# Kernel tuning notes

Hardware: AMD Instinct MI355X
Metric: run time of the kernel (lower is better)

Reference implementation:

```python
import jax, jax.numpy as jnp
import numpy as np
from math import sqrt

B, N, DIM_IN, DIM_K, DIM_V, NH = 4, 1024, 1024, 1024, 1024, 16


def setup_inputs() -> dict:
    key = jax.random.key(0)
    ks = jax.random.split(key, 5)
    x = jax.random.normal(ks[0], (B, N, DIM_IN), dtype=jnp.float32)
    y = jax.random.normal(ks[1], (B, N, DIM_IN), dtype=jnp.float32)
    # nn.Linear weights are (out_features, in_features); xavier-like scale
    s = 1.0 / sqrt(DIM_IN)
    Wq = jax.random.normal(ks[2], (DIM_K, DIM_IN), dtype=jnp.float32) * s
    Wk = jax.random.normal(ks[3], (DIM_K, DIM_IN), dtype=jnp.float32) * s
    Wv = jax.random.normal(ks[4], (DIM_V, DIM_IN), dtype=jnp.float32) * s
    return {"x": x, "y": y, "Wq": Wq, "Wk": Wk, "Wv": Wv}


def reference(x, y, Wq, Wk, Wv):
    b, n, _ = x.shape
    nh = NH
    dk = DIM_K // nh
    dv = DIM_V // nh
    norm = 1.0 / sqrt(dk)
    # project and split heads: (b, h, n, d)
    q = (x @ Wq.T).reshape(b, n, nh, dk).transpose(0, 2, 1, 3)
    k = (x @ Wk.T).reshape(b, n, nh, dk).transpose(0, 2, 1, 3)
    v = (y @ Wv.T).reshape(b, n, nh, dv).transpose(0, 2, 1, 3)
    scores = jnp.einsum("bhnd,bhmd->bhnm", q, k) * norm
    dist = jax.nn.softmax(scores, axis=-1)
    # contrast branch: softmax over (1 - dist)
    dist_a = jax.nn.softmax(1.0 - dist, axis=-1)
    c_att = jnp.einsum("bhnm,bhmd->bhnd", dist_a, v)
    c_att = c_att.transpose(0, 2, 1, 3).reshape(b, n, DIM_V)
    # normal branch: NOTE the original applies softmax to dist AGAIN
    dist2 = jax.nn.softmax(dist, axis=-1)
    att = jnp.einsum("bhnm,bhmd->bhnd", dist2, v)
    att = att.transpose(0, 2, 1, 3).reshape(b, n, DIM_V)
    return (c_att, att)
```

## Files before the change

### kernel.cpp

```cpp
#include <hip/hip_runtime.h>


typedef __attribute__((ext_vector_type(8))) short bf16x8;
typedef __attribute__((ext_vector_type(4))) float f32x4;
typedef __attribute__((ext_vector_type(4))) float float4v;
typedef __attribute__((ext_vector_type(2))) unsigned int uint2v;
typedef __attribute__((ext_vector_type(4))) unsigned short ushort4v;

#define DEVINL static __device__ __forceinline__

DEVINL unsigned f2bf_u(float f) {
  unsigned u = __float_as_uint(f);
  return (u + 0x7fffu + ((u >> 16) & 1u)) >> 16;
}
DEVINL unsigned short f2bf(float f) { return (unsigned short)f2bf_u(f); }
DEVINL unsigned pack2(float lo, float hi) { return f2bf_u(lo) | (f2bf_u(hi) << 16); }

DEVINL unsigned cvtpk(float lo, float hi) {
  unsigned r; asm("v_cvt_pk_bf16_f32 %0, %1, %2" : "=v"(r) : "v"(lo), "v"(hi)); return r;
}

DEVINL float fexp2(float x) {
  float r; asm("v_exp_f32 %0, %1" : "=v"(r) : "v"(x)); return r;
}

DEVINL void gload_lds16(const void* g, void* l) {
  __builtin_amdgcn_global_load_lds((const __attribute__((address_space(1))) unsigned int*)g,
                                   (__attribute__((address_space(3))) unsigned int*)l, 16, 0, 0);
}

DEVINL f32x4 mfma16(bf16x8 a, bf16x8 b, f32x4 c) {
  return __builtin_amdgcn_mfma_f32_16x16x32_bf16(a, b, c, 0, 0, 0);
}

__global__ void cvt_all(const float* __restrict__ x, const float* __restrict__ y,
                        const float* __restrict__ wq, const float* __restrict__ wk,
                        const float* __restrict__ wv,
                        unsigned short* __restrict__ xb, unsigned short* __restrict__ yb,
                        unsigned short* __restrict__ wqb, unsigned short* __restrict__ wkb,
                        unsigned short* __restrict__ wvb) {
  long long e = (long long)blockIdx.x * 2048 + (long long)threadIdx.x * 8;
  const float* s; unsigned short* d; long long off;
  if (e < 4194304)       { s = x;  d = xb;  off = e; }
  else if (e < 8388608)  { s = y;  d = yb;  off = e - 4194304; }
  else if (e < 9437184)  { s = wq; d = wqb; off = e - 8388608; }
  else if (e < 10485760) { s = wk; d = wkb; off = e - 9437184; }
  else                   { s = wv; d = wvb; off = e - 10485760; }
  float4v a = *(const float4v*)(s + off);
  float4v b = *(const float4v*)(s + off + 4);
  ushort4v lo = { f2bf(a[0]), f2bf(a[1]), f2bf(a[2]), f2bf(a[3]) };
  ushort4v hi = { f2bf(b[0]), f2bf(b[1]), f2bf(b[2]), f2bf(b[3]) };
  *(ushort4v*)(d + off) = lo;
  *(ushort4v*)(d + off + 4) = hi;
}

__global__ __launch_bounds__(256, 3)
void gemm_proj(const unsigned short* __restrict__ xb, const unsigned short* __restrict__ yb,
               const unsigned short* __restrict__ wq, const unsigned short* __restrict__ wk,
               const unsigned short* __restrict__ wv,
               unsigned short* __restrict__ Qb, unsigned short* __restrict__ Kb,
               unsigned short* __restrict__ Vt) {
  const int z = blockIdx.z;
  const unsigned short* A  = (z == 2) ? yb : xb;
  const unsigned short* Bw = (z == 0) ? wq : ((z == 1) ? wk : wv);

  __shared__ unsigned short lA[128 * 32];
  __shared__ unsigned short lB[128 * 32];

  const int tid = threadIdx.x;
  const int w = tid >> 6, l = tid & 63;
  const int lq = l & 15, lg = l >> 4;
  const int tm = blockIdx.y, tn = blockIdx.x;

  const int srow = l >> 2;
  const int scol = (l & 3) * 8;
  const size_t arow0 = (size_t)tm * 128 + w * 16 + srow;
  const size_t brow0 = (size_t)tn * 128 + w * 16 + srow;
  const int wr = (w >> 1) * 64, wc = (w & 1) * 64;

  f32x4 zero4 = {0.f, 0.f, 0.f, 0.f};
  f32x4 acc[4][4];
#pragma unroll
  for (int m = 0; m < 4; ++m)
#pragma unroll
    for (int n = 0; n < 4; ++n) acc[m][n] = zero4;

  for (int k0 = 0; k0 < 1024; k0 += 32) {
    gload_lds16(A + arow0 * 1024 + k0 + scol,        &lA[w * 512]);
    gload_lds16(A + (arow0 + 64) * 1024 + k0 + scol, &lA[w * 512 + 2048]);
    gload_lds16(Bw + brow0 * 1024 + k0 + scol,        &lB[w * 512]);
    gload_lds16(Bw + (brow0 + 64) * 1024 + k0 + scol, &lB[w * 512 + 2048]);
    __syncthreads();
    bf16x8 af[4], bfr[4];
#pragma unroll
    for (int m = 0; m < 4; ++m) af[m]  = *(const bf16x8*)&lA[(wr + m * 16 + lq) * 32 + lg * 8];
#pragma unroll
    for (int n = 0; n < 4; ++n) bfr[n] = *(const bf16x8*)&lB[(wc + n * 16 + lq) * 32 + lg * 8];
#pragma unroll
    for (int m = 0; m < 4; ++m)
#pragma unroll
      for (int n = 0; n < 4; ++n)
        acc[m][n] = mfma16(af[m], bfr[n], acc[m][n]);
    __syncthreads();
  }

  if (z < 2) {
    unsigned short* O = (z == 0) ? Qb : Kb;
    const float scale = (z == 0) ? 0.18033688011116012f : 1.0f;
#pragma unroll
    for (int m = 0; m < 4; ++m)
#pragma unroll
      for (int n = 0; n < 4; ++n) {
        int row0 = tm * 128 + wr + m * 16 + lg * 4;
        int col  = tn * 128 + wc + n * 16 + lq;
#pragma unroll
        for (int j = 0; j < 4; ++j)
          O[(size_t)(row0 + j) * 1024 + col] = f2bf(acc[m][n][j] * scale);
      }
  } else {
#pragma unroll
    for (int m = 0; m < 4; ++m)
#pragma unroll
      for (int n = 0; n < 4; ++n) {
        int row0 = tm * 128 + wr + m * 16 + lg * 4;
        int col  = tn * 128 + wc + n * 16 + lq;
        int bb = row0 >> 10, n0 = row0 & 1023;
        uint2v p = { pack2(acc[m][n][0], acc[m][n][1]), pack2(acc[m][n][2], acc[m][n][3]) };
        *(uint2v*)(Vt + ((size_t)(bb * 1024 + col)) * 1024 + n0) = p;
      }
  }
}

DEVINL void stage_tileK(const unsigned short* __restrict__ ghead, int m0,
                        unsigned short* tile, int w, int l) {
#pragma unroll
  for (int i = 0; i < 2; ++i) {
    const int c = i * 256 + w * 64 + l;
    const int row = c >> 3;
    const int col16 = (c & 7) ^ (row & 7);
    gload_lds16(ghead + (size_t)(m0 + row) * 1024 + col16 * 8,
                tile + (size_t)(i * 256 + w * 64) * 8);
  }
}
DEVINL void stage_tileV(const unsigned short* __restrict__ ghead, int m0,
                        unsigned short* tile, int w, int l) {
#pragma unroll
  for (int i = 0; i < 2; ++i) {
    const int c = i * 256 + w * 64 + l;
    const int row = c >> 3;
    const int col16 = (c & 7) ^ (row & 7);
    gload_lds16(ghead + (size_t)row * 1024 + m0 + col16 * 8,
                tile + (size_t)(i * 256 + w * 64) * 8);
  }
}
DEVINL bf16x8 lds_rd(const unsigned short* tile, int r, int g) {
  return *(const bf16x8*)((const char*)tile + (r << 7) + ((g ^ (r & 7)) << 4));
}

__global__ __launch_bounds__(256, 4)
void attn_fused(const unsigned short* __restrict__ Qb, const unsigned short* __restrict__ Kb,
                const unsigned short* __restrict__ Vt, float* __restrict__ out) {
  __shared__ unsigned short Kl[2][4096];
  __shared__ unsigned short Vl[2][4096];
  __shared__ unsigned short Pl[4][1024];

  const int tid = threadIdx.x;
  const int w = tid >> 6, l = tid & 63;
  const int lq = l & 15, lg = l >> 4;

  const int orig = blockIdx.x;
  const int vid = (orig & 7) * 128 + (orig >> 3);
  const int tile = vid & 15;
  const int h = (vid >> 4) & 15;
  const int b = vid >> 8;
  const int qBase = tile * 64 + w * 16;

  const unsigned short* Khead = Kb + ((size_t)b << 20) + h * 64;
  const unsigned short* Vhead = Vt + ((size_t)(b * 1024 + h * 64)) * 1024;
  char* Pb = (char*)&Pl[w][0];

  bf16x8 qf[2];
#pragma unroll
  for (int kst = 0; kst < 2; ++kst)
    qf[kst] = *(const bf16x8*)(Qb + ((size_t)(b * 1024 + qBase + lq)) * 1024
                                  + h * 64 + kst * 32 + lg * 8);

  f32x4 zero4 = {0.f, 0.f, 0.f, 0.f};

  stage_tileK(Khead, 0, Kl[0], w, l);
  __syncthreads();
  float rZ = 0.f;
  for (int mc = 0; mc < 16; ++mc) {
    if (mc < 15) stage_tileK(Khead, (mc + 1) * 64, Kl[(mc + 1) & 1], w, l);
    const unsigned short* Kt = Kl[mc & 1];
#pragma unroll
    for (int sub = 0; sub < 4; ++sub) {
      const int r = sub * 16 + lq;
      bf16x8 ka0 = lds_rd(Kt, r, lg);
      bf16x8 ka1 = lds_rd(Kt, r, 4 + lg);
      f32x4 t = zero4;
      t = mfma16(ka0, qf[0], t);
      t = mfma16(ka1, qf[1], t);
      rZ += (fexp2(t[0]) + fexp2(t[1])) + (fexp2(t[2]) + fexp2(t[3]));
    }
    __syncthreads();
  }

  stage_tileK(Khead, 0, Kl[0], w, l);
  stage_tileV(Vhead, 0, Vl[0], w, l);
  rZ += __shfl_xor(rZ, 16, 64);
  rZ += __shfl_xor(rZ, 32, 64);
  const float cRow = 0.5287663f - __log2f(rZ);
  __syncthreads();

  float Z2 = 0.f, Za = 0.f;
  f32x4 o2[4], oa[4];
#pragma unroll
  for (int dvg = 0; dvg < 4; ++dvg) { o2[dvg] = zero4; oa[dvg] = zero4; }

  for (int mc = 0; mc < 16; ++mc) {
    if (mc < 15) {
      stage_tileK(Khead, (mc + 1) * 64, Kl[(mc + 1) & 1], w, l);
      stage_tileV(Vhead, (mc + 1) * 64, Vl[(mc + 1) & 1], w, l);
    }
    const unsigned short* Kt  = Kl[mc & 1];
    const unsigned short* Vtl = Vl[mc & 1];

#pragma unroll
    for (int sub = 0; sub < 4; ++sub) {
      const int r = sub * 16 + lq;
      bf16x8 ka0 = lds_rd(Kt, r, lg);
      bf16x8 ka1 = lds_rd(Kt, r, 4 + lg);
      f32x4 t = zero4;
      t = mfma16(ka0, qf[0], t);
      t = mfma16(ka1, qf[1], t);
      float w2v[4];
#pragma unroll
      for (int j = 0; j < 4; ++j) {
        float u = fexp2(t[j] + cRow);
        w2v[j] = fexp2(u);
      }
      const int gw = sub * 2 + (lg >> 1);
      char* dst = Pb + lq * 128 + ((gw ^ (lq & 7)) << 4) + ((lg & 1) << 3);
      *(uint2v*)dst = (uint2v){ cvtpk(w2v[0], w2v[1]), cvtpk(w2v[2], w2v[3]) };
    }

#pragma unroll
    for (int kst2 = 0; kst2 < 2; ++kst2) {
      bf16x8 vf[4];
#pragma unroll
      for (int dvg = 0; dvg < 4; ++dvg)
        vf[dvg] = lds_rd(Vtl, dvg * 16 + lq, kst2 * 4 + lg);
      bf16x8 a2 = *(const bf16x8*)(Pb + lq * 128 + (((kst2 * 4 + lg) ^ (lq & 7)) << 4));
      union { bf16x8 h; unsigned u[4]; } ua; ua.h = a2;
      union { unsigned u[4]; bf16x8 h; } ub;
      float zs2 = 0.f, zsa = 0.f;
#pragma unroll
      for (int d = 0; d < 4; ++d) {
        float lo = __uint_as_float(ua.u[d] << 16);
        float hi = __uint_as_float(ua.u[d] & 0xffff0000u);
        float rlo = __builtin_amdgcn_rcpf(lo);
        float rhi = __builtin_amdgcn_rcpf(hi);
        zs2 += lo + hi; zsa += rlo + rhi;
        ub.u[d] = cvtpk(rlo, rhi);
      }
      Z2 += zs2; Za += zsa;
      bf16x8 aav = ub.h;
#pragma unroll
      for (int dvg = 0; dvg < 4; ++dvg) {
        o2[dvg] = mfma16(a2,  vf[dvg], o2[dvg]);
        oa[dvg] = mfma16(aav, vf[dvg], oa[dvg]);
      }
    }
    __syncthreads();
  }

  Z2 += __shfl_xor(Z2, 16, 64); Z2 += __shfl_xor(Z2, 32, 64);
  Za += __shfl_xor(Za, 16, 64); Za += __shfl_xor(Za, 32, 64);
  const float i2 = 1.0f / Z2;
  const float ia = 1.0f / Za;

#pragma unroll
  for (int j = 0; j < 4; ++j) {
    const int src = lg * 4 + j;
    const float z2j = __shfl(i2, src, 64);
    const float zaj = __shfl(ia, src, 64);
    const int nrow = qBase + lg * 4 + j;
    const size_t rb = ((size_t)(b * 1024 + nrow)) * 1024 + h * 64;
#pragma unroll
    for (int dvg = 0; dvg < 4; ++dvg) {
      const int dv = dvg * 16 + lq;
      out[rb + dv] = oa[dvg][j] * zaj;
      out[4194304 + rb + dv] = o2[dvg][j] * z2j;
    }
  }
}

extern "C" void kernel_launch(void* const* d_in, const int* in_sizes, int n_in,
                              void* d_out, int out_size, void* d_ws, size_t ws_size,
                              hipStream_t stream) {
  const float* x  = (const float*)d_in[0];
  const float* y  = (const float*)d_in[1];
  const float* Wq = (const float*)d_in[2];
  const float* Wk = (const float*)d_in[3];
  const float* Wv = (const float*)d_in[4];
  float* out = (float*)d_out;
  char* ws = (char*)d_ws;
  const size_t MB = 1024 * 1024;
  unsigned short* xb  = (unsigned short*)(ws + 0 * MB);
  unsigned short* yb  = (unsigned short*)(ws + 8 * MB);
  unsigned short* wqb = (unsigned short*)(ws + 16 * MB);
  unsigned short* wkb = (unsigned short*)(ws + 18 * MB);
  unsigned short* wvb = (unsigned short*)(ws + 20 * MB);
  unsigned short* Qb  = (unsigned short*)(ws + 22 * MB);
  unsigned short* Kb  = (unsigned short*)(ws + 30 * MB);
  unsigned short* Vt  = (unsigned short*)(ws + 38 * MB);

  cvt_all<<<dim3(5632), dim3(256), 0, stream>>>(x, y, Wq, Wk, Wv, xb, yb, wqb, wkb, wvb);

  gemm_proj<<<dim3(8, 32, 3), dim3(256), 0, stream>>>(xb, yb, wqb, wkb, wvb, Qb, Kb, Vt);

  attn_fused<<<dim3(1024), dim3(256), 0, stream>>>(Qb, Kb, Vt, out);
}
```

Baseline: 106.6 us.

## Cache unnormalized exp scores in registers and replace second QK pass with polynomial

The first pass now keeps all 128 packed bf16 exp(score) values per lane in registers. The second pass reuses them instead of reloading K and redoing the QK MFMAs. The double exp and the reciprocal are replaced by a Taylor polynomial, using cosh+sinh for exp(d) and cosh-sinh for exp(-d) of the normalized probability d. Both weight sets are written to LDS, the K/V buffers are merged, and launch bounds drop to 2 blocks per CU. The risks are register pressure from the 128-entry array (possible spills) and lower occupancy. It also relies on d staying small enough for the truncated series to be accurate.

After: 268.1 us. 2.51x slower.

```diff
diff --git a/kernel.cpp b/kernel.cpp
--- a/kernel.cpp
+++ b/kernel.cpp
@@ -157,12 +157,11 @@
   return *(const bf16x8*)((const char*)tile + (r << 7) + ((g ^ (r & 7)) << 4));
 }
 
-__global__ __launch_bounds__(256, 4)
+__global__ __launch_bounds__(256, 2)
 void attn_fused(const unsigned short* __restrict__ Qb, const unsigned short* __restrict__ Kb,
                 const unsigned short* __restrict__ Vt, float* __restrict__ out) {
-  __shared__ unsigned short Kl[2][4096];
-  __shared__ unsigned short Vl[2][4096];
-  __shared__ unsigned short Pl[4][1024];
+  __shared__ unsigned short Tl[2][4096];
+  __shared__ unsigned short Pl[4][2048];
 
   const int tid = threadIdx.x;
   const int w = tid >> 6, l = tid & 63;
@@ -177,7 +176,8 @@
 
   const unsigned short* Khead = Kb + ((size_t)b << 20) + h * 64;
   const unsigned short* Vhead = Vt + ((size_t)(b * 1024 + h * 64)) * 1024;
-  char* Pb = (char*)&Pl[w][0];
+  char* P2 = (char*)&Pl[w][0];
+  char* Pa = (char*)&Pl[w][1024];
 
   bf16x8 qf[2];
 #pragma unroll
@@ -187,12 +187,14 @@
 
   f32x4 zero4 = {0.f, 0.f, 0.f, 0.f};
 
-  stage_tileK(Khead, 0, Kl[0], w, l);
+  unsigned ez[128];
+  stage_tileK(Khead, 0, Tl[0], w, l);
   __syncthreads();
   float rZ = 0.f;
+#pragma unroll
   for (int mc = 0; mc < 16; ++mc) {
-    if (mc < 15) stage_tileK(Khead, (mc + 1) * 64, Kl[(mc + 1) & 1], w, l);
-    const unsigned short* Kt = Kl[mc & 1];
+    if (mc < 15) stage_tileK(Khead, (mc + 1) * 64, Tl[(mc + 1) & 1], w, l);
+    const unsigned short* Kt = Tl[mc & 1];
 #pragma unroll
     for (int sub = 0; sub < 4; ++sub) {
       const int r = sub * 16 + lq;
@@ -201,16 +203,18 @@
       f32x4 t = zero4;
       t = mfma16(ka0, qf[0], t);
       t = mfma16(ka1, qf[1], t);
-      rZ += (fexp2(t[0]) + fexp2(t[1])) + (fexp2(t[2]) + fexp2(t[3]));
+      float e0 = fexp2(t[0]), e1 = fexp2(t[1]), e2 = fexp2(t[2]), e3 = fexp2(t[3]);
+      rZ += (e0 + e1) + (e2 + e3);
+      ez[mc * 8 + sub * 2 + 0] = cvtpk(e0, e1);
+      ez[mc * 8 + sub * 2 + 1] = cvtpk(e2, e3);
     }
     __syncthreads();
   }
 
-  stage_tileK(Khead, 0, Kl[0], w, l);
-  stage_tileV(Vhead, 0, Vl[0], w, l);
+  stage_tileV(Vhead, 0, Tl[0], w, l);
   rZ += __shfl_xor(rZ, 16, 64);
   rZ += __shfl_xor(rZ, 32, 64);
-  const float cRow = 0.5287663f - __log2f(rZ);
+  const float invZ = 1.0f / rZ;
   __syncthreads();
 
   float Z2 = 0.f, Za = 0.f;
@@ -218,54 +222,48 @@
 #pragma unroll
   for (int dvg = 0; dvg < 4; ++dvg) { o2[dvg] = zero4; oa[dvg] = zero4; }
 
+#pragma unroll
   for (int mc = 0; mc < 16; ++mc) {
-    if (mc < 15) {
-      stage_tileK(Khead, (mc + 1) * 64, Kl[(mc + 1) & 1], w, l);
-      stage_tileV(Vhead, (mc + 1) * 64, Vl[(mc + 1) & 1], w, l);
+    if (mc < 15) stage_tileV(Vhead, (mc + 1) * 64, Tl[(mc + 1) & 1], w, l);
+
+#pragma unroll
+    for (int sub = 0; sub < 4; ++sub) {
+      const unsigned p0 = ez[mc * 8 + sub * 2 + 0];
+      const unsigned p1 = ez[mc * 8 + sub * 2 + 1];
+      float dv4[4];
+      dv4[0] = __uint_as_float(p0 << 16) * invZ;
+      dv4[1] = __uint_as_float(p0 & 0xffff0000u) * invZ;
+      dv4[2] = __uint_as_float(p1 << 16) * invZ;
+      dv4[3] = __uint_as_float(p1 & 0xffff0000u) * invZ;
+      float w2v[4], wav[4];
+      float zs2 = 0.f, zsa = 0.f;
+#pragma unroll
+      for (int j = 0; j < 4; ++j) {
+        const float d = dv4[j];
+        const float x2 = d * d;
+        const float c = fmaf(fmaf(fmaf(x2, 1.388888889e-3f, 4.166666667e-2f), x2, 0.5f), x2, 1.0f);
+        const float s = fmaf(fmaf(x2, 8.333333333e-3f, 0.16666667f), x2, 1.0f) * d;
+        w2v[j] = c + s;
+        wav[j] = c - s;
+        zs2 += w2v[j]; zsa += wav[j];
+      }
+      Z2 += zs2; Za += zsa;
+      const int gw = sub * 2 + (lg >> 1);
+      const int boff = lq * 128 + ((gw ^ (lq & 7)) << 4) + ((lg & 1) << 3);
+      *(uint2v*)(P2 + boff) = (uint2v){ cvtpk(w2v[0], w2v[1]), cvtpk(w2v[2], w2v[3]) };
+      *(uint2v*)(Pa + boff) = (uint2v){ cvtpk(wav[0], wav[1]), cvtpk(wav[2], wav[3]) };
     }
-    const unsigned short* Kt  = Kl[mc & 1];
-    const unsigned short* Vtl = Vl[mc & 1];
-
-#pragma unroll
-    for (int sub = 0; sub < 4; ++sub) {
-      const int r = sub * 16 + lq;
-      bf16x8 ka0 = lds_rd(Kt, r, lg);
-      bf16x8 ka1 = lds_rd(Kt, r, 4 + lg);
-      f32x4 t = zero4;
-      t = mfma16(ka0, qf[0], t);
-      t = mfma16(ka1, qf[1], t);
-      float w2v[4];
-#pragma unroll
-      for (int j = 0; j < 4; ++j) {
-        float u = fexp2(t[j] + cRow);
-        w2v[j] = fexp2(u);
-      }
-      const int gw = sub * 2 + (lg >> 1);
-      char* dst = Pb + lq * 128 + ((gw ^ (lq & 7)) << 4) + ((lg & 1) << 3);
-      *(uint2v*)dst = (uint2v){ cvtpk(w2v[0], w2v[1]), cvtpk(w2v[2], w2v[3]) };
-    }
-
+
+    const unsigned short* Vtl = Tl[mc & 1];
 #pragma unroll
     for (int kst2 = 0; kst2 < 2; ++kst2) {
       bf16x8 vf[4];
 #pragma unroll
       for (int dvg = 0; dvg < 4; ++dvg)
         vf[dvg] = lds_rd(Vtl, dvg * 16 + lq, kst2 * 4 + lg);
-      bf16x8 a2 = *(const bf16x8*)(Pb + lq * 128 + (((kst2 * 4 + lg) ^ (lq & 7)) << 4));
-      union { bf16x8 h; unsigned u[4]; } ua; ua.h = a2;
-      union { unsigned u[4]; bf16x8 h; } ub;
-      float zs2 = 0.f, zsa = 0.f;
-#pragma unroll
-      for (int d = 0; d < 4; ++d) {
-        float lo = __uint_as_float(ua.u[d] << 16);
-        float hi = __uint_as_float(ua.u[d] & 0xffff0000u);
-        float rlo = __builtin_amdgcn_rcpf(lo);
-        float rhi = __builtin_amdgcn_rcpf(hi);
-        zs2 += lo + hi; zsa += rlo + rhi;
-        ub.u[d] = cvtpk(rlo, rhi);
-      }
-      Z2 += zs2; Za += zsa;
-      bf16x8 aav = ub.h;
+      const int roff = lq * 128 + (((kst2 * 4 + lg) ^ (lq & 7)) << 4);
+      bf16x8 a2  = *(const bf16x8*)(P2 + roff);
+      bf16x8 aav = *(const bf16x8*)(Pa + roff);
 #pragma unroll
       for (int dvg = 0; dvg < 4; ++dvg) {
         o2[dvg] = mfma16(a2,  vf[dvg], o2[dvg]);
```
